# Kernel tuning notes

Measured on AMD Instinct MI355X. Metric: run time of the kernel, lower is better.

The kernel has to match this reference:

```python
import jax, jax.numpy as jnp
import numpy as np

B, T, D = 8, 2048, 1024
DK, DV = 1024, 1024


def setup_inputs() -> dict:
    key = jax.random.key(0)
    ks = jax.random.split(key, 7)
    s = 1.0 / np.sqrt(D)
    return {
        "X": jax.random.normal(ks[0], (B, T, D), dtype=jnp.float32),
        "Wq": jax.random.uniform(ks[1], (D, DK), jnp.float32, -s, s),
        "bq": jax.random.uniform(ks[2], (DK,), jnp.float32, -s, s),
        "Wk": jax.random.uniform(ks[3], (D, DK), jnp.float32, -s, s),
        "bk": jax.random.uniform(ks[4], (DK,), jnp.float32, -s, s),
        "Wv": jax.random.uniform(ks[5], (D, DV), jnp.float32, -s, s),
        "bv": jax.random.uniform(ks[6], (DV,), jnp.float32, -s, s),
    }


def reference(X, Wq, bq, Wk, bk, Wv, bv):
    # relu-activated projections (note: original applies relu to Q, K, V; no 1/sqrt(d) scaling)
    Q = jax.nn.relu(jnp.einsum("btd,dk->btk", X, Wq) + bq)  # [B,T,DK]
    K = jax.nn.relu(jnp.einsum("btd,dk->btk", X, Wk) + bk)  # [B,T,DK]
    V = jax.nn.relu(jnp.einsum("btd,dv->btv", X, Wv) + bv)  # [B,T,DV]
    scores = jnp.einsum("btk,bsk->bts", Q, K)               # [B,T,S] query t attends over keys s
    attn = jax.nn.softmax(scores, axis=-1)
    return jnp.einsum("bts,bsv->btv", attn, V)              # [B,T,DV]
```

## Files before the change

### kernel.cpp

```cpp
#include <hip/hip_runtime.h>

typedef __bf16 bf16x8 __attribute__((ext_vector_type(8)));
typedef _Float16 f16x8 __attribute__((ext_vector_type(8)));
typedef float floatx4 __attribute__((ext_vector_type(4)));

__device__ __forceinline__ unsigned short f2bf(float f) {
  unsigned int u = __float_as_uint(f);
  u += 0x7FFFu + ((u >> 16) & 1u);
  return (unsigned short)(u >> 16);
}
__device__ __forceinline__ unsigned short f2h(float f) {
  _Float16 h = (_Float16)f;
  return __builtin_bit_cast(unsigned short, h);
}
template <bool F16>
__device__ __forceinline__ unsigned short f2x(float f) {
  return F16 ? f2h(f) : f2bf(f);
}
__device__ __forceinline__ unsigned short f2rt(float f, bool f16) {
  return f16 ? f2h(f) : f2bf(f);
}

__device__ __forceinline__ void g2l16(const void* g, void* l) {
  __builtin_amdgcn_global_load_lds(
      (const __attribute__((address_space(1))) void*)g,
      (__attribute__((address_space(3))) void*)l, 16, 0, 0);
}

template <int MODE, bool AF32, bool INF16, bool OUTF16, bool PROJ3>
__global__ __launch_bounds__(256) void gemm_bt(
    const void* __restrict__ Av, int lda, long sA,
    const unsigned short* __restrict__ B, int ldb, long sB,
    void* __restrict__ Cv, int ldc, long sC,
    int K, const float* __restrict__ bias, float* __restrict__ lrow,
    void* __restrict__ C1, void* __restrict__ C2) {
  __shared__ unsigned short As[2][128 * 64];
  __shared__ unsigned short Bs[2][128 * 64];
  const int tid = threadIdx.x;
  const int wave = tid >> 6, lane = tid & 63;
  const int z = blockIdx.z;
  const unsigned short* A16 = (const unsigned short*)Av + (size_t)z * sA;
  const float* A32 = (const float*)Av + (size_t)z * sA;
  B += (size_t)z * sB;

  void* Cz = Cv;
  const float* biasz = bias;
  bool outf16 = OUTF16;
  if (PROJ3) {
    biasz = bias + z * 1024;
    if (z == 1) Cz = C1;
    else if (z == 2) { Cz = C2; outf16 = false; }
  }

  int bx = blockIdx.x, by = blockIdx.y;
  {
    const int nwg = gridDim.x * gridDim.y;
    if ((nwg & 7) == 0) {
      int flat = by * gridDim.x + bx;
      flat = (flat & 7) * (nwg >> 3) + (flat >> 3);
      bx = flat % gridDim.x;
      by = flat / gridDim.x;
    }
  }
  const int m0 = by * 128, n0 = bx * 128;
  const int wr = (wave >> 1) * 64;
  const int wc = (wave & 1) * 64;
  const int qr = lane >> 4, lr = lane & 15;
  floatx4 acc[4][4] = {};

  auto stageAB = [&](int t, int buf) {
    const int k0 = t << 6;
#pragma unroll
    for (int it = 0; it < 4; ++it) {
      const int base = it * 256 + wave * 64;
      const int idx = base + lane;
      const int row = idx >> 3;
      const int gs = (idx & 7) ^ (row & 7);
      g2l16(A16 + (size_t)(m0 + row) * lda + k0 + gs * 8, &As[buf][base * 8]);
    }
#pragma unroll
    for (int it = 0; it < 4; ++it) {
      const int base = it * 256 + wave * 64;
      const int idx = base + lane;
      const int row = idx >> 3;
      const int gs = (idx & 7) ^ (row & 7);
      g2l16(B + (size_t)(n0 + row) * ldb + k0 + gs * 8, &Bs[buf][base * 8]);
    }
  };

  auto computeT = [&](int buf) {
#pragma unroll
    for (int kk = 0; kk < 64; kk += 32) {
      const int slot = (kk >> 3) + qr;
      if (INF16) {
        f16x8 af[4], bf[4];
#pragma unroll
        for (int i = 0; i < 4; ++i) {
          const int ra = wr + i * 16 + lr;
          af[i] = *(const f16x8*)&As[buf][ra * 64 + ((slot ^ (ra & 7)) * 8)];
        }
#pragma unroll
        for (int j = 0; j < 4; ++j) {
          const int rb = wc + j * 16 + lr;
          bf[j] = *(const f16x8*)&Bs[buf][rb * 64 + ((slot ^ (rb & 7)) * 8)];
        }
#pragma unroll
        for (int i = 0; i < 4; ++i)
#pragma unroll
          for (int j = 0; j < 4; ++j)
            acc[i][j] = __builtin_amdgcn_mfma_f32_16x16x32_f16(
                bf[j], af[i], acc[i][j], 0, 0, 0);
      } else {
        bf16x8 af[4], bf[4];
#pragma unroll
        for (int i = 0; i < 4; ++i) {
          const int ra = wr + i * 16 + lr;
          af[i] = *(const bf16x8*)&As[buf][ra * 64 + ((slot ^ (ra & 7)) * 8)];
        }
#pragma unroll
        for (int j = 0; j < 4; ++j) {
          const int rb = wc + j * 16 + lr;
          bf[j] = *(const bf16x8*)&Bs[buf][rb * 64 + ((slot ^ (rb & 7)) * 8)];
        }
#pragma unroll
        for (int i = 0; i < 4; ++i)
#pragma unroll
          for (int j = 0; j < 4; ++j)
            acc[i][j] = __builtin_amdgcn_mfma_f32_16x16x32_bf16(
                bf[j], af[i], acc[i][j], 0, 0, 0);
      }
    }
  };

  if (!AF32) {
    const int nk = K >> 6;
    stageAB(0, 0);
    for (int t = 0; t < nk; ++t) {
      const int cur = t & 1;
      if (t + 1 < nk) {
        stageAB(t + 1, cur ^ 1);
        asm volatile("s_waitcnt vmcnt(8)" ::: "memory");
      } else {
        asm volatile("s_waitcnt vmcnt(0)" ::: "memory");
      }
      __builtin_amdgcn_sched_barrier(0);
      __builtin_amdgcn_s_barrier();
      __builtin_amdgcn_sched_barrier(0);
      computeT(cur);
      __builtin_amdgcn_sched_barrier(0);
      __builtin_amdgcn_s_barrier();
      __builtin_amdgcn_sched_barrier(0);
    }
  } else {
    for (int k0 = 0; k0 < K; k0 += 64) {
      __syncthreads();
#pragma unroll
      for (int it = 0; it < 8; ++it) {
        const int idx = it * 256 + tid;
        const int row = idx >> 4, c4 = idx & 15;
        float4 v =
            *(const float4*)(A32 + (size_t)(m0 + row) * lda + k0 + c4 * 4);
        const int soff = (((c4 >> 1) ^ (row & 7)) * 2 + (c4 & 1)) * 4;
        *(ushort4*)&As[0][row * 64 + soff] =
            make_ushort4(f2x<INF16>(v.x), f2x<INF16>(v.y), f2x<INF16>(v.z),
                         f2x<INF16>(v.w));
      }
#pragma unroll
      for (int it = 0; it < 4; ++it) {
        const int base = it * 256 + wave * 64;
        const int idx = base + lane;
        const int row = idx >> 3;
        const int gs = (idx & 7) ^ (row & 7);
        g2l16(B + (size_t)(n0 + row) * ldb + k0 + gs * 8, &Bs[0][base * 8]);
      }
      __syncthreads();
      computeT(0);
    }
  }

  float* Cf = (float*)Cz + (size_t)z * sC;
  unsigned short* Cb = (unsigned short*)Cz + (size_t)z * sC;
#pragma unroll
  for (int i = 0; i < 4; ++i) {
    const int row = m0 + wr + i * 16 + lr;
    float rowsum = 0.0f;
    float invl = 1.0f;
    if (MODE == 2) invl = 1.0f / lrow[(size_t)z * 2048 + row];
#pragma unroll
    for (int j = 0; j < 4; ++j) {
      const int col0 = n0 + wc + j * 16 + qr * 4;
      if (MODE == 0) {
        float4 bj = *(const float4*)(biasz + col0);
        float v0 = fmaxf(acc[i][j][0] + bj.x, 0.0f);
        float v1 = fmaxf(acc[i][j][1] + bj.y, 0.0f);
        float v2 = fmaxf(acc[i][j][2] + bj.z, 0.0f);
        float v3 = fmaxf(acc[i][j][3] + bj.w, 0.0f);
        *(ushort4*)&Cb[(size_t)row * ldc + col0] =
            make_ushort4(f2rt(v0, outf16), f2rt(v1, outf16),
                         f2rt(v2, outf16), f2rt(v3, outf16));
      } else if (MODE == 1) {
        float e0 = __expf(acc[i][j][0] - 60.0f);
        float e1 = __expf(acc[i][j][1] - 60.0f);
        float e2 = __expf(acc[i][j][2] - 60.0f);
        float e3 = __expf(acc[i][j][3] - 60.0f);
        *(ushort4*)&Cb[(size_t)row * ldc + col0] =
            make_ushort4(f2bf(e0), f2bf(e1), f2bf(e2), f2bf(e3));
        rowsum += (e0 + e1) + (e2 + e3);
      } else {
        *(float4*)&Cf[(size_t)row * ldc + col0] =
            make_float4(acc[i][j][0] * invl, acc[i][j][1] * invl,
                        acc[i][j][2] * invl, acc[i][j][3] * invl);
      }
    }
    if (MODE == 1) {
      rowsum += __shfl_xor(rowsum, 16);
      rowsum += __shfl_xor(rowsum, 32);
      if (lane < 16)
        atomicAdd(&lrow[(size_t)z * 2048 + row], rowsum);
    }
  }
}

__global__ __launch_bounds__(256) void prep(
    const float* __restrict__ X, unsigned short* __restrict__ Xh,
    const float* __restrict__ Wq, const float* __restrict__ Wk,
    const float* __restrict__ Wv, unsigned short* __restrict__ Wqt,
    unsigned short* __restrict__ Wkt, unsigned short* __restrict__ Wvt,
    const float* __restrict__ bq, const float* __restrict__ bk,
    const float* __restrict__ bv, float* __restrict__ bcat,
    float* __restrict__ l) {
  __shared__ unsigned short t[64][68];
  const int bid = blockIdx.x;
  const int tid = threadIdx.x;
  if (bid < 8192) {
    const int i = (bid * 256 + tid) * 8;
    float4 a = *(const float4*)(X + i);
    float4 b = *(const float4*)(X + i + 4);
    *(ushort4*)(Xh + i) = make_ushort4(f2h(a.x), f2h(a.y), f2h(a.z), f2h(a.w));
    *(ushort4*)(Xh + i + 4) =
        make_ushort4(f2h(b.x), f2h(b.y), f2h(b.z), f2h(b.w));
  } else if (bid < 8960) {
    const int w = (bid - 8192) >> 8;
    const int lb = (bid - 8192) & 255;
    const float* W = (w == 0) ? Wq : (w == 1) ? Wk : Wv;
    unsigned short* Wt = (w == 0) ? Wqt : (w == 1) ? Wkt : Wvt;
    const int n0 = (lb & 15) * 64, k0 = (lb >> 4) * 64;
#pragma unroll
    for (int it = 0; it < 4; ++it) {
      const int idx = it * 256 + tid;
      const int kr = idx >> 4, nq = idx & 15;
      float4 v = *(const float4*)&W[(size_t)(k0 + kr) * 1024 + n0 + nq * 4];
      t[kr][nq * 4 + 0] = f2h(v.x);
      t[kr][nq * 4 + 1] = f2h(v.y);
      t[kr][nq * 4 + 2] = f2h(v.z);
      t[kr][nq * 4 + 3] = f2h(v.w);
    }
    __syncthreads();
#pragma unroll
    for (int it = 0; it < 4; ++it) {
      const int idx = it * 256 + tid;
      const int nr = idx >> 4, kq = idx & 15;
      *(ushort4*)&Wt[(size_t)(n0 + nr) * 1024 + k0 + kq * 4] =
          make_ushort4(t[kq * 4 + 0][nr], t[kq * 4 + 1][nr],
                       t[kq * 4 + 2][nr], t[kq * 4 + 3][nr]);
    }
  } else if (bid < 9024) {
    const int i = (bid - 8960) * 256 + tid;
    l[i] = 0.0f;
  } else {
#pragma unroll
    for (int it = 0; it < 12; ++it) {
      const int idx = it * 256 + tid;
      bcat[idx] = (idx < 1024) ? bq[idx]
                  : (idx < 2048) ? bk[idx - 1024] : bv[idx - 2048];
    }
  }
}

__global__ __launch_bounds__(256) void vtrans(const unsigned short* __restrict__ V,
                                              unsigned short* __restrict__ Vt) {
  __shared__ unsigned short t[64][68];
  const int tid = threadIdx.x;
  const int v0 = blockIdx.x * 64, t0 = blockIdx.y * 64;
  const int b = blockIdx.z;
  const unsigned short* Vb = V + (size_t)b * 2048 * 1024;
  unsigned short* Vtb = Vt + (size_t)b * 1024 * 2048;
#pragma unroll
  for (int it = 0; it < 4; ++it) {
    const int idx = it * 256 + tid;
    const int tr = idx >> 4, vq = idx & 15;
    ushort4 u = *(const ushort4*)&Vb[(size_t)(t0 + tr) * 1024 + v0 + vq * 4];
    t[tr][vq * 4 + 0] = u.x;
    t[tr][vq * 4 + 1] = u.y;
    t[tr][vq * 4 + 2] = u.z;
    t[tr][vq * 4 + 3] = u.w;
  }
  __syncthreads();
#pragma unroll
  for (int it = 0; it < 4; ++it) {
    const int idx = it * 256 + tid;
    const int vr = idx >> 4, tq = idx & 15;
    *(ushort4*)&Vtb[(size_t)(v0 + vr) * 2048 + t0 + tq * 4] =
        make_ushort4(t[tq * 4 + 0][vr], t[tq * 4 + 1][vr],
                     t[tq * 4 + 2][vr], t[tq * 4 + 3][vr]);
  }
}

__global__ __launch_bounds__(256) void copy_half(const float* __restrict__ T,
                                                 float* __restrict__ out,
                                                 int roff) {
  const size_t i = ((size_t)blockIdx.x * 256 + threadIdx.x) * 4;
  const size_t b = i >> 20;
  const size_t rem = i & 1048575;
  float4 v = *(const float4*)(T + i);
  *(float4*)(out + b * 2097152 + (size_t)roff * 1024 + rem) = v;
}

__global__ void diag_ws(float* __restrict__ out, float mb) { out[0] = mb; }

extern "C" void kernel_launch(void* const* d_in, const int* in_sizes, int n_in,
                              void* d_out, int out_size, void* d_ws, size_t ws_size,
                              hipStream_t stream) {
  const float* X = (const float*)d_in[0];
  const float* Wq = (const float*)d_in[1];
  const float* bq = (const float*)d_in[2];
  const float* Wk = (const float*)d_in[3];
  const float* bk = (const float*)d_in[4];
  const float* Wv = (const float*)d_in[5];
  const float* bv = (const float*)d_in[6];
  float* out = (float*)d_out;
  char* ws = (char*)d_ws;
  const size_t MiB = 1ull << 20;

  const size_t B_WQT = 0, B_WKT = 2 * MiB, B_WVT = 4 * MiB;
  const size_t B_Q = 6 * MiB;
  const size_t B_K = 38 * MiB;
  const size_t B_E = 70 * MiB;
  const size_t B_L = 134 * MiB;
  const size_t NEEDED_BIG = B_L + 65536 + 16384;

  const size_t S_WQT = 0, S_WKT = 2 * MiB, S_WVT = 4 * MiB;
  const size_t S_Q = 6 * MiB, S_K = 38 * MiB, S_L = 70 * MiB;
  const size_t NEEDED_SMALL = S_L + 65536 + 16384;

  if (ws_size >= NEEDED_BIG) {
    unsigned short* Wqt = (unsigned short*)(ws + B_WQT);
    unsigned short* Wkt = (unsigned short*)(ws + B_WKT);
    unsigned short* Wvt = (unsigned short*)(ws + B_WVT);
    unsigned short* Q   = (unsigned short*)(ws + B_Q);
    unsigned short* Kb  = (unsigned short*)(ws + B_K);
    unsigned short* E   = (unsigned short*)(ws + B_E);
    float* l            = (float*)(ws + B_L);
    float* bcat         = (float*)(ws + B_L + 65536);
    unsigned short* Xh = (unsigned short*)d_out;
    unsigned short* V  = (unsigned short*)d_out + 16384ull * 1024;

    prep<<<9025, 256, 0, stream>>>(X, Xh, Wq, Wk, Wv, Wqt, Wkt, Wvt,
                                   bq, bk, bv, bcat, l);

    gemm_bt<0, false, true, true, true><<<dim3(8, 128, 3), 256, 0, stream>>>(
        Xh, 1024, 0, Wqt, 1024, 1048576, Q, 1024, 0, 1024, bcat, nullptr,
        Kb, V);

    gemm_bt<1, false, true, false, false><<<dim3(16, 16, 8), 256, 0, stream>>>(
        Q, 1024, 2048L * 1024, Kb, 1024, 2048L * 1024,
        E, 2048, 2048L * 2048, 1024, nullptr, l, nullptr, nullptr);

    vtrans<<<dim3(16, 32, 8), 256, 0, stream>>>(V, Q);

    gemm_bt<2, false, false, false, false><<<dim3(8, 16, 8), 256, 0, stream>>>(
        E, 2048, 2048L * 2048, Q, 2048, 1024L * 2048,
        out, 1024, 2048L * 1024, 2048, nullptr, l, nullptr, nullptr);
    return;
  }

  if (ws_size < NEEDED_SMALL) {
    diag_ws<<<1, 1, 0, stream>>>(out, (float)(ws_size >> 20));
    return;
  }

  unsigned short* Wqt = (unsigned short*)(ws + S_WQT);
  unsigned short* Wkt = (unsigned short*)(ws + S_WKT);
  unsigned short* Wvt = (unsigned short*)(ws + S_WVT);
  unsigned short* Q   = (unsigned short*)(ws + S_Q);
  unsigned short* Kb  = (unsigned short*)(ws + S_K);
  float* l            = (float*)(ws + S_L);
  float* bcat         = (float*)(ws + S_L + 65536);
  unsigned short* Xh = (unsigned short*)d_out;
  unsigned short* E  = (unsigned short*)d_out;

  prep<<<9025, 256, 0, stream>>>(X, Xh, Wq, Wk, Wv, Wqt, Wkt, Wvt,
                                 bq, bk, bv, bcat, l);

  gemm_bt<0, false, true, true, true><<<dim3(8, 128, 2), 256, 0, stream>>>(
      Xh, 1024, 0, Wqt, 1024, 1048576, Q, 1024, 0, 1024, bcat, nullptr,
      Kb, nullptr);

  gemm_bt<1, false, true, false, false><<<dim3(16, 16, 8), 256, 0, stream>>>(
      Q, 1024, 2048L * 1024, Kb, 1024, 2048L * 1024,
      E, 2048, 2048L * 2048, 1024, nullptr, l, nullptr, nullptr);

  gemm_bt<0, true, true, false, false><<<dim3(8, 128, 1), 256, 0, stream>>>(
      X, 1024, 0, Wvt, 1024, 0, Kb, 1024, 0, 1024, bv, nullptr,
      nullptr, nullptr);

  vtrans<<<dim3(16, 32, 8), 256, 0, stream>>>(Kb, Q);

  float* T = (float*)Kb;
  gemm_bt<2, false, false, false, false><<<dim3(8, 8, 8), 256, 0, stream>>>(
      E, 2048, 2048L * 2048, Q, 2048, 1024L * 2048,
      T, 1024, 1024L * 1024, 2048, nullptr, l, nullptr, nullptr);
  copy_half<<<8192, 256, 0, stream>>>(T, out, 0);
  gemm_bt<2, false, false, false, false><<<dim3(8, 8, 8), 256, 0, stream>>>(
      E + 1024L * 2048, 2048, 2048L * 2048, Q, 2048, 1024L * 2048,
      T, 1024, 1024L * 1024, 2048, nullptr, l + 1024, nullptr, nullptr);
  copy_half<<<8192, 256, 0, stream>>>(T, out, 1024);
}
```

Measured before the change: 440.7 us.

## Fuse V transpose into projection GEMM epilogue, drop vtrans kernel

The V projection slice now swaps the MFMA operands so each lane holds consecutive time rows. It writes V already transposed ([v][t], bf16) straight from the epilogue, which removes the separate vtrans kernel and its extra read/write of V. V^T lives in the upper half of the output buffer, so the final E·V GEMM now writes batches 4-7 to a workspace buffer, and a new flat copy kernel moves them into the output afterward. It also wraps the MFMA blocks in s_setprio raises. The cost is strided stores in the transposed epilogue plus an extra 32 MiB copy.

Result: slower. 585.2 us (+32.8%).

```diff
diff --git a/kernel.cpp b/kernel.cpp
--- a/kernel.cpp
+++ b/kernel.cpp
@@ -46,6 +46,7 @@
   void* Cz = Cv;
   const float* biasz = bias;
   bool outf16 = OUTF16;
+  const bool zV = PROJ3 && (z == 2);
   if (PROJ3) {
     biasz = bias + z * 1024;
     if (z == 1) Cz = C1;
@@ -104,12 +105,23 @@
           const int rb = wc + j * 16 + lr;
           bf[j] = *(const f16x8*)&Bs[buf][rb * 64 + ((slot ^ (rb & 7)) * 8)];
         }
-#pragma unroll
-        for (int i = 0; i < 4; ++i)
-#pragma unroll
-          for (int j = 0; j < 4; ++j)
-            acc[i][j] = __builtin_amdgcn_mfma_f32_16x16x32_f16(
-                bf[j], af[i], acc[i][j], 0, 0, 0);
+        __builtin_amdgcn_s_setprio(1);
+        if (zV) {
+#pragma unroll
+          for (int i = 0; i < 4; ++i)
+#pragma unroll
+            for (int j = 0; j < 4; ++j)
+              acc[i][j] = __builtin_amdgcn_mfma_f32_16x16x32_f16(
+                  af[i], bf[j], acc[i][j], 0, 0, 0);
+        } else {
+#pragma unroll
+          for (int i = 0; i < 4; ++i)
+#pragma unroll
+            for (int j = 0; j < 4; ++j)
+              acc[i][j] = __builtin_amdgcn_mfma_f32_16x16x32_f16(
+                  bf[j], af[i], acc[i][j], 0, 0, 0);
+        }
+        __builtin_amdgcn_s_setprio(0);
       } else {
         bf16x8 af[4], bf[4];
 #pragma unroll
@@ -122,12 +134,14 @@
           const int rb = wc + j * 16 + lr;
           bf[j] = *(const bf16x8*)&Bs[buf][rb * 64 + ((slot ^ (rb & 7)) * 8)];
         }
+        __builtin_amdgcn_s_setprio(1);
 #pragma unroll
         for (int i = 0; i < 4; ++i)
 #pragma unroll
           for (int j = 0; j < 4; ++j)
             acc[i][j] = __builtin_amdgcn_mfma_f32_16x16x32_bf16(
                 bf[j], af[i], acc[i][j], 0, 0, 0);
+        __builtin_amdgcn_s_setprio(0);
       }
     }
   };
@@ -178,7 +192,31 @@
     }
   }
 
+  if (zV) {
+    unsigned short* Vt = (unsigned short*)Cz;
+#pragma unroll
+    for (int i = 0; i < 4; ++i) {
+      const int trow0 = m0 + wr + i * 16 + qr * 4;
+      const size_t vb = (size_t)(trow0 >> 11) * (1024ull * 2048);
+      const int tt = trow0 & 2047;
+#pragma unroll
+      for (int j = 0; j < 4; ++j) {
+        const int vcol = n0 + wc + j * 16 + lr;
+        const float bvv = biasz[vcol];
+        float v0 = fmaxf(acc[i][j][0] + bvv, 0.0f);
+        float v1 = fmaxf(acc[i][j][1] + bvv, 0.0f);
+        float v2 = fmaxf(acc[i][j][2] + bvv, 0.0f);
+        float v3 = fmaxf(acc[i][j][3] + bvv, 0.0f);
+        *(ushort4*)&Vt[vb + (size_t)vcol * 2048 + tt] =
+            make_ushort4(f2bf(v0), f2bf(v1), f2bf(v2), f2bf(v3));
+      }
+    }
+    return;
+  }
+
   float* Cf = (float*)Cz + (size_t)z * sC;
+  if (MODE == 2 && C1 != nullptr && z >= 4)
+    Cf = (float*)C1 + (size_t)(z - 4) * sC;
   unsigned short* Cb = (unsigned short*)Cz + (size_t)z * sC;
 #pragma unroll
   for (int i = 0; i < 4; ++i) {
@@ -306,6 +344,12 @@
   }
 }
 
+__global__ __launch_bounds__(256) void copyflat(const float* __restrict__ src,
+                                                float* __restrict__ dst) {
+  const size_t i = ((size_t)blockIdx.x * 256 + threadIdx.x) * 4;
+  *(float4*)(dst + i) = *(const float4*)(src + i);
+}
+
 __global__ __launch_bounds__(256) void copy_half(const float* __restrict__ T,
                                                  float* __restrict__ out,
                                                  int roff) {
@@ -353,24 +397,25 @@
     float* l            = (float*)(ws + B_L);
     float* bcat         = (float*)(ws + B_L + 65536);
     unsigned short* Xh = (unsigned short*)d_out;
-    unsigned short* V  = (unsigned short*)d_out + 16384ull * 1024;
+    unsigned short* Vt = (unsigned short*)d_out + 16384ull * 1024;
 
     prep<<<9025, 256, 0, stream>>>(X, Xh, Wq, Wk, Wv, Wqt, Wkt, Wvt,
                                    bq, bk, bv, bcat, l);
 
     gemm_bt<0, false, true, true, true><<<dim3(8, 128, 3), 256, 0, stream>>>(
         Xh, 1024, 0, Wqt, 1024, 1048576, Q, 1024, 0, 1024, bcat, nullptr,
-        Kb, V);
+        Kb, Vt);
 
     gemm_bt<1, false, true, false, false><<<dim3(16, 16, 8), 256, 0, stream>>>(
         Q, 1024, 2048L * 1024, Kb, 1024, 2048L * 1024,
         E, 2048, 2048L * 2048, 1024, nullptr, l, nullptr, nullptr);
 
-    vtrans<<<dim3(16, 32, 8), 256, 0, stream>>>(V, Q);
-
+    float* T = (float*)Q;
     gemm_bt<2, false, false, false, false><<<dim3(8, 16, 8), 256, 0, stream>>>(
-        E, 2048, 2048L * 2048, Q, 2048, 1024L * 2048,
-        out, 1024, 2048L * 1024, 2048, nullptr, l, nullptr, nullptr);
+        E, 2048, 2048L * 2048, Vt, 2048, 1024L * 2048,
+        out, 1024, 2048L * 1024, 2048, nullptr, l, T, nullptr);
+
+    copyflat<<<8192, 256, 0, stream>>>(T, out + 4ull * 2048 * 1024);
     return;
   }
 
```
